# Kernel tuning notes

Hardware: AMD Instinct MI355X
Metric: run time of the kernel (lower is better)

Reference implementation:

```python
import jax, jax.numpy as jnp
import numpy as np

P = 100   # num_proxies
N = 1024  # num_samples
D = 512


def _edge_index():
    # complete bipartite proxy<->sample graph, both directions, plus self-loops
    # (PyG GATConv adds self-loops for all nodes by default)
    p = np.arange(P)
    s = np.arange(P, P + N)
    src_ps = np.repeat(p, N)   # proxy -> sample
    dst_ps = np.tile(s, P)
    loops = np.arange(P + N)
    src = np.concatenate([src_ps, dst_ps, loops]).astype(np.int32)
    dst = np.concatenate([dst_ps, src_ps, loops]).astype(np.int32)
    return jnp.asarray(src), jnp.asarray(dst)


def setup_inputs() -> dict:
    key = jax.random.key(0)
    ks = jax.random.split(key, 10)
    sc = 1.0 / np.sqrt(D)
    src, dst = _edge_index()
    return {
        "x": jax.random.normal(ks[0], (N, D), jnp.float32),
        "proxies": jax.random.normal(ks[1], (P, D), jnp.float32),
        "W1": jax.random.normal(ks[2], (D, D), jnp.float32) * sc,
        "a_src1": jax.random.normal(ks[3], (D,), jnp.float32) * sc,
        "a_dst1": jax.random.normal(ks[4], (D,), jnp.float32) * sc,
        "b1": jnp.zeros((D,), jnp.float32),
        "W2": jax.random.normal(ks[5], (D, D), jnp.float32) * sc,
        "a_src2": jax.random.normal(ks[6], (D,), jnp.float32) * sc,
        "a_dst2": jax.random.normal(ks[7], (D,), jnp.float32) * sc,
        "b2": jnp.zeros((D,), jnp.float32),
        "fc_w": jax.random.normal(ks[8], (D, 100), jnp.float32) * sc,
        "fc_b": jnp.zeros((100,), jnp.float32),
        "src": src,
        "dst": dst,
    }


def _gat_conv(x, src, dst, W, a_src, a_dst, b, n_nodes):
    # PyG GATConv, heads=1, concat=True, negative_slope=0.2
    h = x @ W                      # [n, D]
    l_src = h @ a_src              # [n]
    l_dst = h @ a_dst              # [n]
    e = jax.nn.leaky_relu(l_src[src] + l_dst[dst], 0.2)   # [E]
    # segment softmax over edges sharing the same destination
    e = e - jax.ops.segment_max(e, dst, num_segments=n_nodes)[dst]
    ex = jnp.exp(e)
    denom = jax.ops.segment_sum(ex, dst, num_segments=n_nodes)[dst]
    alpha = ex / denom             # [E]
    out = jax.ops.segment_sum(alpha[:, None] * h[src], dst, num_segments=n_nodes)
    return out + b


def reference(x, proxies, W1, a_src1, a_dst1, b1, W2, a_src2, a_dst2, b2, fc_w, fc_b, src, dst):
    n = P + N
    h = jnp.concatenate([proxies, x], axis=0)          # [P+N, D]
    h = jax.nn.relu(_gat_conv(h, src, dst, W1, a_src1, a_dst1, b1, n))
    # Dropout -> identity (eval)
    h = jax.nn.relu(_gat_conv(h, src, dst, W2, a_src2, a_dst2, b2, n))
    preds = h @ fc_w + fc_b                            # [P+N, 100]
    return preds[P:], h[P:]
```

## Files before the change

kernel.cpp:

```cpp
#include <hip/hip_runtime.h>

#define PP 100
#define NS 1024
#define NN 1124
#define DD 512
#define CC 100
#define NTHR 256

typedef _Float16 f16;
typedef _Float16 f16x8 __attribute__((ext_vector_type(8)));
typedef float    f32x4 __attribute__((ext_vector_type(4)));

__device__ __forceinline__ float lk(float v) { return v > 0.f ? v : 0.2f * v; }
__device__ __forceinline__ f16 hif(float v) { return (f16)v; }
__device__ __forceinline__ f16 lof(float v) { return (f16)(v - (float)((f16)v)); }

__device__ __forceinline__ void mgemm_core(
    const f16* __restrict__ Ah, const f16* __restrict__ Al,
    const f16* __restrict__ Bth, const f16* __restrict__ Btl,
    int K, int row0, int col0, f16* __restrict__ lds, f32x4 acc[2][2])
{
  const int t = threadIdx.x;
  const int lane = t & 63, w = t >> 6;
  const int wr = w >> 1, wc = w & 1;
  f16* Ash = lds;
  f16* Asl = lds + 2560;
  f16* Bsh = lds + 5120;
  f16* Bsl = lds + 7680;
  const int srow = t >> 2, su = t & 3;
  const size_t aoff = (size_t)(row0 + srow) * K + su * 8;
  const size_t boff = (size_t)(col0 + srow) * K + su * 8;
  const int lw = srow * 40 + su * 8;
  f32x4 pa0 = *(const f32x4*)(Ah + aoff);
  f32x4 pa1 = *(const f32x4*)(Al + aoff);
  f32x4 pb0 = *(const f32x4*)(Bth + boff);
  f32x4 pb1 = *(const f32x4*)(Btl + boff);
  const int fra = wr * 32 + (lane & 15);
  const int frb = wc * 32 + (lane & 15);
  const int fu  = (lane >> 4) * 8;
  for (int kt = 32; kt <= K; kt += 32) {
    *(f32x4*)(Ash + lw) = pa0;
    *(f32x4*)(Asl + lw) = pa1;
    *(f32x4*)(Bsh + lw) = pb0;
    *(f32x4*)(Bsl + lw) = pb1;
    __syncthreads();
    if (kt < K) {
      pa0 = *(const f32x4*)(Ah + aoff + kt);
      pa1 = *(const f32x4*)(Al + aoff + kt);
      pb0 = *(const f32x4*)(Bth + boff + kt);
      pb1 = *(const f32x4*)(Btl + boff + kt);
    }
    f16x8 ah[2], al[2], bh[2], bl[2];
#pragma unroll
    for (int m = 0; m < 2; ++m) {
      ah[m] = *(const f16x8*)(Ash + (fra + m * 16) * 40 + fu);
      al[m] = *(const f16x8*)(Asl + (fra + m * 16) * 40 + fu);
    }
#pragma unroll
    for (int n = 0; n < 2; ++n) {
      bh[n] = *(const f16x8*)(Bsh + (frb + n * 16) * 40 + fu);
      bl[n] = *(const f16x8*)(Bsl + (frb + n * 16) * 40 + fu);
    }
#pragma unroll
    for (int m = 0; m < 2; ++m)
#pragma unroll
      for (int n = 0; n < 2; ++n) {
        acc[m][n] = __builtin_amdgcn_mfma_f32_16x16x32_f16(ah[m], bh[n], acc[m][n], 0, 0, 0);
        acc[m][n] = __builtin_amdgcn_mfma_f32_16x16x32_f16(al[m], bh[n], acc[m][n], 0, 0, 0);
        acc[m][n] = __builtin_amdgcn_mfma_f32_16x16x32_f16(ah[m], bl[n], acc[m][n], 0, 0, 0);
      }
    __syncthreads();
  }
}


__device__ __forceinline__ void cvt_tile(
    const float* __restrict__ in, int R, int Cin,
    f16* __restrict__ oh, f16* __restrict__ ol, int ldo,
    int ti, int tj, f16 (*th)[72], f16 (*tl)[72])
{
  const int t = threadIdx.x;
#pragma unroll
  for (int p = 0; p < 4; ++p) {
    const int f = t + p * 256;
    const int i = f >> 4, j4 = (f & 15) * 4;
    const int gi = ti * 64 + i, gj = tj * 64 + j4;
    float4 v = make_float4(0.f, 0.f, 0.f, 0.f);
    if (gi < R && gj + 3 < Cin) v = *(const float4*)(in + (size_t)gi * Cin + gj);
    th[i][j4 + 0] = hif(v.x); tl[i][j4 + 0] = lof(v.x);
    th[i][j4 + 1] = hif(v.y); tl[i][j4 + 1] = lof(v.y);
    th[i][j4 + 2] = hif(v.z); tl[i][j4 + 2] = lof(v.z);
    th[i][j4 + 3] = hif(v.w); tl[i][j4 + 3] = lof(v.w);
  }
  __syncthreads();
#pragma unroll
  for (int p = 0; p < 2; ++p) {
    const int f = t + p * 256;
    const int j = f >> 3, i8 = (f & 7) * 8;
    f16x8 vh, vl;
#pragma unroll
    for (int e = 0; e < 8; ++e) { vh[e] = th[i8 + e][j]; vl[e] = tl[i8 + e][j]; }
    const size_t o = (size_t)(tj * 64 + j) * ldo + ti * 64 + i8;
    *(f16x8*)(oh + o) = vh;
    *(f16x8*)(ol + o) = vl;
  }
}

__global__ __launch_bounds__(NTHR) void prep_k(
    const float* __restrict__ x, const float* __restrict__ prox,
    const float* __restrict__ W1, const float* __restrict__ W2,
    const float* __restrict__ fcw,
    const float* __restrict__ as1, const float* __restrict__ ad1,
    const float* __restrict__ as2, const float* __restrict__ ad2,
    f16* xth, f16* xtl, f16* pth, f16* ptl,
    f16* W1th, f16* W1tl, f16* W2th, f16* W2tl, f16* fwth, f16* fwtl,
    float* v1s, float* v1d, float* v2s, float* v2d)
{
  __shared__ f16 th[64][72];
  __shared__ f16 tl[64][72];
  const int b = blockIdx.x;
  if (b < 64) {
    cvt_tile(W1, 512, 512, W1th, W1tl, 512, b >> 3, b & 7, th, tl);
  } else if (b < 128) {
    cvt_tile(W2, 512, 512, W2th, W2tl, 512, (b - 64) >> 3, (b - 64) & 7, th, tl);
  } else if (b < 256) {
    cvt_tile(x, NS, 512, xth, xtl, NS, (b - 128) >> 3, (b - 128) & 7, th, tl);
  } else if (b < 272) {
    cvt_tile(prox, PP, 512, pth, ptl, 128, (b - 256) >> 3, (b - 256) & 7, th, tl);
  } else if (b < 288) {
    cvt_tile(fcw, 512, CC, fwth, fwtl, 512, (b - 272) >> 1, (b - 272) & 1, th, tl);
  } else {
    const int wid  = (b - 288) * 4 + (threadIdx.x >> 6);
    const int lane = threadIdx.x & 63;
    const int r = wid & 511;
    const bool l1 = (wid < 512);
    const float* W = l1 ? W1 : W2;
    const float4* a4 = (const float4*)(l1 ? as1 : as2);
    const float4* b4 = (const float4*)(l1 ? ad1 : ad2);
    const float4* w4 = (const float4*)(W + (size_t)r * DD);
    float4 w0 = w4[lane], w1 = w4[lane + 64];
    float4 a0 = a4[lane], a1 = a4[lane + 64];
    float4 b0 = b4[lane], b1 = b4[lane + 64];
    float s1 = w0.x * a0.x + w0.y * a0.y + w0.z * a0.z + w0.w * a0.w
             + w1.x * a1.x + w1.y * a1.y + w1.z * a1.z + w1.w * a1.w;
    float s2 = w0.x * b0.x + w0.y * b0.y + w0.z * b0.z + w0.w * b0.w
             + w1.x * b1.x + w1.y * b1.y + w1.z * b1.z + w1.w * b1.w;
#pragma unroll
    for (int off = 32; off > 0; off >>= 1) {
      s1 += __shfl_down(s1, off);
      s2 += __shfl_down(s2, off);
    }
    if (lane == 0) {
      (l1 ? v1s : v2s)[r] = s1;
      (l1 ? v1d : v2d)[r] = s2;
    }
  }
}

__global__ __launch_bounds__(NTHR) void lvec_k(
    const float* __restrict__ A0, const float* __restrict__ A1, int split,
    const float* __restrict__ vs, const float* __restrict__ vd,
    float* __restrict__ ls, float* __restrict__ ld)
{
  const int r    = blockIdx.x * 4 + (threadIdx.x >> 6);
  const int lane = threadIdx.x & 63;
  if (r >= NN) return;
  const float* row = (r < split) ? A0 + (size_t)r * DD : A1 + (size_t)(r - split) * DD;
  const float4* r4 = (const float4*)row;
  const float4* s4 = (const float4*)vs;
  const float4* d4 = (const float4*)vd;
  float4 v0 = r4[lane], v1 = r4[lane + 64];
  float4 a0 = s4[lane], a1 = s4[lane + 64];
  float4 b0 = d4[lane], b1 = d4[lane + 64];
  float s1 = v0.x * a0.x + v0.y * a0.y + v0.z * a0.z + v0.w * a0.w
           + v1.x * a1.x + v1.y * a1.y + v1.z * a1.z + v1.w * a1.w;
  float s2 = v0.x * b0.x + v0.y * b0.y + v0.z * b0.z + v0.w * b0.w
           + v1.x * b1.x + v1.y * b1.y + v1.z * b1.z + v1.w * b1.w;
#pragma unroll
  for (int off = 32; off > 0; off >>= 1) {
    s1 += __shfl_down(s1, off);
    s2 += __shfl_down(s2, off);
  }
  if (lane == 0) { ls[r] = s1; ld[r] = s2; }
}

__global__ __launch_bounds__(NTHR) void alpha_k(
    const float* __restrict__ ls, const float* __restrict__ ld,
    f16* __restrict__ Esh, f16* __restrict__ Esl,
    float* __restrict__ esS, float* __restrict__ izS,
    f16* __restrict__ Eph, f16* __restrict__ Epl,
    float* __restrict__ esP, float* __restrict__ izP)
{
  const int t = threadIdx.x;
  if (blockIdx.x < 256) {
    const int lane = t & 63;
    const int i = blockIdx.x * 4 + (t >> 6);
    const float ldi = ld[PP + i];
    float e0 = lk(ls[lane] + ldi);
    float e1 = (lane < PP - 64) ? lk(ls[lane + 64] + ldi) : -1e30f;
    const float eself = lk(ls[PP + i] + ldi);
    float m = fmaxf(fmaxf(e0, e1), eself);
#pragma unroll
    for (int off = 1; off < 64; off <<= 1) m = fmaxf(m, __shfl_xor(m, off));
    float x0 = __expf(e0 - m);
    float x1 = (lane < PP - 64) ? __expf(e1 - m) : 0.f;
    float z = x0 + x1;
#pragma unroll
    for (int off = 1; off < 64; off <<= 1) z += __shfl_xor(z, off);
    Esh[(size_t)i * 128 + lane]      = hif(x0);
    Esl[(size_t)i * 128 + lane]      = lof(x0);
    Esh[(size_t)i * 128 + 64 + lane] = hif(x1);
    Esl[(size_t)i * 128 + 64 + lane] = lof(x1);
    if (lane == 0) {
      float xs = __expf(eself - m);
      esS[i] = xs;
      izS[i] = 1.f / (z + xs);
    }
  } else {
    const int i = blockIdx.x - 256;
    if (i >= PP) {
#pragma unroll
      for (int q = 0; q < 4; ++q) {
        Eph[(size_t)i * NS + t + q * 256] = (f16)0.f;
        Epl[(size_t)i * NS + t + q * 256] = (f16)0.f;
      }
      return;
    }
    __shared__ float red[4];
    const float ldi = ld[i];
    const float eself = lk(ls[i] + ldi);
    float e[4];
#pragma unroll
    for (int q = 0; q < 4; ++q) e[q] = lk(ls[PP + t + q * 256] + ldi);
    float m = fmaxf(fmaxf(fmaxf(e[0], e[1]), fmaxf(e[2], e[3])), eself);
#pragma unroll
    for (int off = 1; off < 64; off <<= 1) m = fmaxf(m, __shfl_xor(m, off));
    if ((t & 63) == 0) red[t >> 6] = m;
    __syncthreads();
    m = fmaxf(fmaxf(red[0], red[1]), fmaxf(red[2], red[3]));
    __syncthreads();
    float xq[4], z = 0.f;
#pragma unroll
    for (int q = 0; q < 4; ++q) { xq[q] = __expf(e[q] - m); z += xq[q]; }
#pragma unroll
    for (int off = 1; off < 64; off <<= 1) z += __shfl_xor(z, off);
    if ((t & 63) == 0) red[t >> 6] = z;
    __syncthreads();
#pragma unroll
    for (int q = 0; q < 4; ++q) {
      Eph[(size_t)i * NS + t + q * 256] = hif(xq[q]);
      Epl[(size_t)i * NS + t + q * 256] = lof(xq[q]);
    }
    if (t == 0) {
      float xs = __expf(eself - m);
      esP[i] = xs;
      izP[i] = 1.f / (red[0] + red[1] + red[2] + red[3] + xs);
    }
  }
}

__global__ __launch_bounds__(NTHR) void agg1_k(
    const f16* __restrict__ Es1h, const f16* __restrict__ Es1l,
    const f16* __restrict__ pth,  const f16* __restrict__ ptl,
    const f16* __restrict__ Eph,  const f16* __restrict__ Epl,
    const f16* __restrict__ xth,  const f16* __restrict__ xtl,
    const float* __restrict__ x, const float* __restrict__ prox,
    const float* __restrict__ esS, const float* __restrict__ izS,
    const float* __restrict__ esP, const float* __restrict__ izP,
    f16* __restrict__ M1h, f16* __restrict__ M1l)
{
  __shared__ __align__(16) f16 lds[10240];
  f32x4 acc[2][2] = {};
  const int t = threadIdx.x, lane = t & 63, w = t >> 6, wr = w >> 1, wc = w & 1;
  const int b = blockIdx.x;
  if (b < 128) {
    const int row0 = (b >> 3) * 64, col0 = (b & 7) * 64;
    mgemm_core(Es1h, Es1l, pth, ptl, 128, row0, col0, lds, acc);
#pragma unroll
    for (int m = 0; m < 2; ++m)
#pragma unroll
      for (int q = 0; q < 4; ++q) {
        const int r = row0 + wr * 32 + m * 16 + (lane >> 4) * 4 + q;
        const float e = esS[r], z = izS[r];
#pragma unroll
        for (int n = 0; n < 2; ++n) {
          const int c = col0 + wc * 32 + n * 16 + (lane & 15);
          const float v = (acc[m][n][q] + e * x[(size_t)r * DD + c]) * z;
          const size_t o = (size_t)(PP + r) * DD + c;
          M1h[o] = hif(v); M1l[o] = lof(v);
        }
      }
  } else {
    const int b2 = b - 128;
    const int row0 = (b2 >> 3) * 64, col0 = (b2 & 7) * 64;
    mgemm_core(Eph, Epl, xth, xtl, NS, row0, col0, lds, acc);
#pragma unroll
    for (int m = 0; m < 2; ++m)
#pragma unroll
      for (int q = 0; q < 4; ++q) {
        const int r = row0 + wr * 32 + m * 16 + (lane >> 4) * 4 + q;
        if (r < PP) {
          const float e = esP[r], z = izP[r];
#pragma unroll
          for (int n = 0; n < 2; ++n) {
            const int c = col0 + wc * 32 + n * 16 + (lane & 15);
            const float v = (acc[m][n][q] + e * prox[(size_t)r * DD + c]) * z;
            const size_t o = (size_t)r * DD + c;
            M1h[o] = hif(v); M1l[o] = lof(v);
          }
        }
      }
  }
}

__global__ __launch_bounds__(NTHR) void h1_k(
    const f16* __restrict__ M1h, const f16* __restrict__ M1l,
    const f16* __restrict__ W1th, const f16* __restrict__ W1tl,
    const float* __restrict__ b1, float* __restrict__ h1,
    f16* __restrict__ h1pth, f16* __restrict__ h1ptl)
{
  __shared__ __align__(16) f16 lds[10240];
  f32x4 acc[2][2] = {};
  const int t = threadIdx.x, lane = t & 63, w = t >> 6, wr = w >> 1, wc = w & 1;
  const int b = blockIdx.x;
  const int row0 = (b >> 3) * 64, col0 = (b & 7) * 64;
  mgemm_core(M1h, M1l, W1th, W1tl, DD, row0, col0, lds, acc);
#pragma unroll
  for (int m = 0; m < 2; ++m)
#pragma unroll
    for (int q = 0; q < 4; ++q) {
      const int r = row0 + wr * 32 + m * 16 + (lane >> 4) * 4 + q;
      if (r >= NN) continue;
#pragma unroll
      for (int n = 0; n < 2; ++n) {
        const int c = col0 + wc * 32 + n * 16 + (lane & 15);
        const float v = fmaxf(acc[m][n][q] + b1[c], 0.f);
        h1[(size_t)r * DD + c] = v;
        if (r < 128) {
          const size_t o = (size_t)c * 128 + r;
          f16 hh = (f16)0.f, ll = (f16)0.f;
          if (r < PP) { hh = hif(v); ll = lof(v); }
          h1pth[o] = hh; h1ptl[o] = ll;
        }
      }
    }
}

__global__ __launch_bounds__(NTHR) void agg2_k(
    const f16* __restrict__ Es2h, const f16* __restrict__ Es2l,
    const f16* __restrict__ h1pth, const f16* __restrict__ h1ptl,
    const float* __restrict__ h1,
    const float* __restrict__ esS, const float* __restrict__ izS,
    f16* __restrict__ M2h, f16* __restrict__ M2l)
{
  __shared__ __align__(16) f16 lds[10240];
  f32x4 acc[2][2] = {};
  const int t = threadIdx.x, lane = t & 63, w = t >> 6, wr = w >> 1, wc = w & 1;
  const int b = blockIdx.x;
  const int row0 = (b >> 3) * 64, col0 = (b & 7) * 64;
  mgemm_core(Es2h, Es2l, h1pth, h1ptl, 128, row0, col0, lds, acc);
#pragma unroll
  for (int m = 0; m < 2; ++m)
#pragma unroll
    for (int q = 0; q < 4; ++q) {
      const int r = row0 + wr * 32 + m * 16 + (lane >> 4) * 4 + q;
      const float e = esS[r], z = izS[r];
#pragma unroll
      for (int n = 0; n < 2; ++n) {
        const int c = col0 + wc * 32 + n * 16 + (lane & 15);
        const float v = (acc[m][n][q] + e * h1[(size_t)(PP + r) * DD + c]) * z;
        const size_t o = (size_t)r * DD + c;
        M2h[o] = hif(v); M2l[o] = lof(v);
      }
    }
}

__global__ __launch_bounds__(NTHR) void h2_k(
    const f16* __restrict__ M2h, const f16* __restrict__ M2l,
    const f16* __restrict__ W2th, const f16* __restrict__ W2tl,
    const float* __restrict__ b2, float* __restrict__ h2s,
    f16* __restrict__ h2h, f16* __restrict__ h2l)
{
  __shared__ __align__(16) f16 lds[10240];
  f32x4 acc[2][2] = {};
  const int t = threadIdx.x, lane = t & 63, w = t >> 6, wr = w >> 1, wc = w & 1;
  const int b = blockIdx.x;
  const int row0 = (b >> 3) * 64, col0 = (b & 7) * 64;
  mgemm_core(M2h, M2l, W2th, W2tl, DD, row0, col0, lds, acc);
#pragma unroll
  for (int m = 0; m < 2; ++m)
#pragma unroll
    for (int q = 0; q < 4; ++q) {
      const int r = row0 + wr * 32 + m * 16 + (lane >> 4) * 4 + q;
#pragma unroll
      for (int n = 0; n < 2; ++n) {
        const int c = col0 + wc * 32 + n * 16 + (lane & 15);
        const float v = fmaxf(acc[m][n][q] + b2[c], 0.f);
        const size_t o = (size_t)r * DD + c;
        h2s[o] = v;
        h2h[o] = hif(v); h2l[o] = lof(v);
      }
    }
}

__global__ __launch_bounds__(NTHR) void fc_k(
    const f16* __restrict__ h2h, const f16* __restrict__ h2l,
    const f16* __restrict__ fwth, const f16* __restrict__ fwtl,
    const float* __restrict__ fcb, float* __restrict__ out)
{
  __shared__ __align__(16) f16 lds[10240];
  f32x4 acc[2][2] = {};
  const int t = threadIdx.x, lane = t & 63, w = t >> 6, wr = w >> 1, wc = w & 1;
  const int b = blockIdx.x;
  const int row0 = (b >> 1) * 64, col0 = (b & 1) * 64;
  mgemm_core(h2h, h2l, fwth, fwtl, DD, row0, col0, lds, acc);
#pragma unroll
  for (int m = 0; m < 2; ++m)
#pragma unroll
    for (int q = 0; q < 4; ++q) {
      const int r = row0 + wr * 32 + m * 16 + (lane >> 4) * 4 + q;
#pragma unroll
      for (int n = 0; n < 2; ++n) {
        const int c = col0 + wc * 32 + n * 16 + (lane & 15);
        if (c < CC) out[(size_t)r * CC + c] = acc[m][n][q] + fcb[c];
      }
    }
}

extern "C" void kernel_launch(void* const* d_in, const int* in_sizes, int n_in,
                              void* d_out, int out_size, void* d_ws, size_t ws_size,
                              hipStream_t stream)
{
  const float* x    = (const float*)d_in[0];
  const float* prox = (const float*)d_in[1];
  const float* W1   = (const float*)d_in[2];
  const float* as1  = (const float*)d_in[3];
  const float* ad1  = (const float*)d_in[4];
  const float* b1   = (const float*)d_in[5];
  const float* W2   = (const float*)d_in[6];
  const float* as2  = (const float*)d_in[7];
  const float* ad2  = (const float*)d_in[8];
  const float* b2   = (const float*)d_in[9];
  const float* fcw  = (const float*)d_in[10];
  const float* fcb  = (const float*)d_in[11];
  float* out = (float*)d_out;

  float* F = (float*)d_ws;
  float* h1   = F; F += (size_t)NN * DD;
  float* ls1  = F; F += 1152;
  float* ld1  = F; F += 1152;
  float* ls2  = F; F += 1152;
  float* ld2  = F; F += 1152;
  float* v1s  = F; F += DD;
  float* v1d  = F; F += DD;
  float* v2s  = F; F += DD;
  float* v2d  = F; F += DD;
  float* esS1 = F; F += NS;
  float* izS1 = F; F += NS;
  float* esS2 = F; F += NS;
  float* izS2 = F; F += NS;
  float* esP  = F; F += 128;
  float* izP  = F; F += 128;
  f16* H = (f16*)F;
  f16* M1h  = H; H += (size_t)1152 * DD;
  f16* M1l  = H; H += (size_t)1152 * DD;
  f16* M2h  = H; H += (size_t)NS * DD;
  f16* M2l  = H; H += (size_t)NS * DD;
  f16* Es1h = H; H += (size_t)NS * 128;
  f16* Es1l = H; H += (size_t)NS * 128;
  f16* Es2h = H; H += (size_t)NS * 128;
  f16* Es2l = H; H += (size_t)NS * 128;
  f16* Eph  = H; H += (size_t)128 * NS;
  f16* Epl  = H; H += (size_t)128 * NS;
  f16* xth  = H; H += (size_t)DD * NS;
  f16* xtl  = H; H += (size_t)DD * NS;
  f16* pth  = H; H += (size_t)DD * 128;
  f16* ptl  = H; H += (size_t)DD * 128;
  f16* W1th = H; H += (size_t)DD * DD;
  f16* W1tl = H; H += (size_t)DD * DD;
  f16* W2th = H; H += (size_t)DD * DD;
  f16* W2tl = H; H += (size_t)DD * DD;
  f16* fwth = H; H += (size_t)128 * DD;
  f16* fwtl = H; H += (size_t)128 * DD;
  f16* h2h  = H; H += (size_t)NS * DD;
  f16* h2l  = H; H += (size_t)NS * DD;
  f16* h1pth = H; H += (size_t)DD * 128;
  f16* h1ptl = H; H += (size_t)DD * 128;
  float* h2s = out + (size_t)NS * CC;

  dim3 blk(NTHR);
  prep_k<<<dim3(544), blk, 0, stream>>>(x, prox, W1, W2, fcw, as1, ad1, as2, ad2,
      xth, xtl, pth, ptl, W1th, W1tl, W2th, W2tl, fwth, fwtl,
      v1s, v1d, v2s, v2d);
  lvec_k<<<dim3(281), blk, 0, stream>>>(prox, x, PP, v1s, v1d, ls1, ld1);
  alpha_k<<<dim3(256 + 128), blk, 0, stream>>>(ls1, ld1, Es1h, Es1l, esS1, izS1,
                                               Eph, Epl, esP, izP);
  agg1_k<<<dim3(144), blk, 0, stream>>>(Es1h, Es1l, pth, ptl, Eph, Epl, xth, xtl,
                                        x, prox, esS1, izS1, esP, izP, M1h, M1l);
  h1_k<<<dim3(144), blk, 0, stream>>>(M1h, M1l, W1th, W1tl, b1, h1, h1pth, h1ptl);
  lvec_k<<<dim3(281), blk, 0, stream>>>(h1, h1, NN, v2s, v2d, ls2, ld2);
  alpha_k<<<dim3(256), blk, 0, stream>>>(ls2, ld2, Es2h, Es2l, esS2, izS2,
                                         Eph, Epl, esP, izP);
  agg2_k<<<dim3(128), blk, 0, stream>>>(Es2h, Es2l, h1pth, h1ptl, h1,
                                        esS2, izS2, M2h, M2l);
  h2_k<<<dim3(128), blk, 0, stream>>>(M2h, M2l, W2th, W2tl, b2, h2s, h2h, h2l);
  fc_k<<<dim3(32), blk, 0, stream>>>(h2h, h2l, fwth, fwtl, fcb, out);
}
```

Baseline: 158.9 us.

## Fuse attention softmax into aggregation GEMMs and attention logits into GEMM epilogue

Removes the separate lvec and alpha kernels. Attention exponentials are now computed on the fly inside the aggregation GEMM's A-tile staging, using a global max bound instead of the exact per-row max. The layer-2 source and destination logits are accumulated in h1_k's epilogue via atomics, and the layer-1 logits are computed inside the prep kernel, which splits prep into two launches. This cuts launch count from 10 to 7 and drops the intermediate E matrices. In exchange it recomputes exp per block and adds atomic float adds, whose summation order is nondeterministic.

```diff
diff --git a/kernel.cpp b/kernel.cpp
--- a/kernel.cpp
+++ b/kernel.cpp
@@ -73,6 +73,121 @@
   }
 }
 
+__device__ __forceinline__ void agg_core(
+    const float* __restrict__ lsrc, int kvalid,
+    const float* __restrict__ ldb, const float* __restrict__ lsb,
+    const f16* __restrict__ Bth, const f16* __restrict__ Btl,
+    int K, int row0, int col0, int rvalid,
+    const float* __restrict__ selfv,
+    f16* __restrict__ outh, f16* __restrict__ outl,
+    f16* __restrict__ lds, float* __restrict__ fred)
+{
+  const int t = threadIdx.x, lane = t & 63, w = t >> 6;
+  const int wr = w >> 1, wc = w & 1;
+  f16* Ash = lds;
+  f16* Asl = lds + 2560;
+  f16* Bsh = lds + 5120;
+  f16* Bsl = lds + 7680;
+  float* zred = fred;
+  float* res  = fred + 256;
+  float* riz  = fred + 320;
+  const int srow = t >> 2, su = t & 3;
+  float sm = -1e30f;
+  for (int k = t; k < kvalid; k += NTHR) sm = fmaxf(sm, lsrc[k]);
+#pragma unroll
+  for (int off = 1; off < 64; off <<= 1) sm = fmaxf(sm, __shfl_xor(sm, off));
+  if (lane == 0) zred[w] = sm;
+  __syncthreads();
+  sm = fmaxf(fmaxf(zred[0], zred[1]), fmaxf(zred[2], zred[3]));
+  __syncthreads();
+  const bool rok = (row0 + srow) < rvalid;
+  float ldr = 0.f, mr = 0.f;
+  if (rok) {
+    ldr = ldb[row0 + srow];
+    mr  = lk(fmaxf(sm, lsb[row0 + srow]) + ldr);
+  }
+  const size_t boff = (size_t)(col0 + srow) * K + su * 8;
+  const int lw = srow * 40 + su * 8;
+  f32x4 pb0 = *(const f32x4*)(Bth + boff);
+  f32x4 pb1 = *(const f32x4*)(Btl + boff);
+  const int fra = wr * 32 + (lane & 15);
+  const int frb = wc * 32 + (lane & 15);
+  const int fu  = (lane >> 4) * 8;
+  f32x4 acc[2][2] = {};
+  float zacc = 0.f;
+  for (int kt = 32; kt <= K; kt += 32) {
+    f16x8 ae, al8;
+    const int k0 = kt - 32 + su * 8;
+#pragma unroll
+    for (int j = 0; j < 8; ++j) {
+      const int k = k0 + j;
+      float f = 0.f;
+      if (rok && k < kvalid) f = __expf(lk(lsrc[k] + ldr) - mr);
+      zacc += f;
+      ae[j]  = hif(f);
+      al8[j] = lof(f);
+    }
+    *(f16x8*)(Ash + lw) = ae;
+    *(f16x8*)(Asl + lw) = al8;
+    *(f32x4*)(Bsh + lw) = pb0;
+    *(f32x4*)(Bsl + lw) = pb1;
+    __syncthreads();
+    if (kt < K) {
+      pb0 = *(const f32x4*)(Bth + boff + kt);
+      pb1 = *(const f32x4*)(Btl + boff + kt);
+    }
+    f16x8 ah[2], alr[2], bh[2], bl[2];
+#pragma unroll
+    for (int m = 0; m < 2; ++m) {
+      ah[m]  = *(const f16x8*)(Ash + (fra + m * 16) * 40 + fu);
+      alr[m] = *(const f16x8*)(Asl + (fra + m * 16) * 40 + fu);
+    }
+#pragma unroll
+    for (int n = 0; n < 2; ++n) {
+      bh[n] = *(const f16x8*)(Bsh + (frb + n * 16) * 40 + fu);
+      bl[n] = *(const f16x8*)(Bsl + (frb + n * 16) * 40 + fu);
+    }
+#pragma unroll
+    for (int m = 0; m < 2; ++m)
+#pragma unroll
+      for (int n = 0; n < 2; ++n) {
+        acc[m][n] = __builtin_amdgcn_mfma_f32_16x16x32_f16(ah[m],  bh[n], acc[m][n], 0, 0, 0);
+        acc[m][n] = __builtin_amdgcn_mfma_f32_16x16x32_f16(alr[m], bh[n], acc[m][n], 0, 0, 0);
+        acc[m][n] = __builtin_amdgcn_mfma_f32_16x16x32_f16(ah[m],  bl[n], acc[m][n], 0, 0, 0);
+      }
+    __syncthreads();
+  }
+  zred[t] = zacc;
+  __syncthreads();
+  if (t < 64) {
+    float z = zred[t * 4] + zred[t * 4 + 1] + zred[t * 4 + 2] + zred[t * 4 + 3];
+    float es = 0.f, iz = 0.f;
+    if (row0 + t < rvalid) {
+      const float l2 = ldb[row0 + t], s2 = lsb[row0 + t];
+      const float m2 = lk(fmaxf(sm, s2) + l2);
+      es = __expf(lk(s2 + l2) - m2);
+      iz = 1.f / (z + es);
+    }
+    res[t] = es; riz[t] = iz;
+  }
+  __syncthreads();
+#pragma unroll
+  for (int m = 0; m < 2; ++m)
+#pragma unroll
+    for (int q = 0; q < 4; ++q) {
+      const int rl = wr * 32 + m * 16 + (lane >> 4) * 4 + q;
+      const int gr = row0 + rl;
+      if (gr >= rvalid) continue;
+      const float es = res[rl], iz = riz[rl];
+#pragma unroll
+      for (int n = 0; n < 2; ++n) {
+        const int c = col0 + wc * 32 + n * 16 + (lane & 15);
+        const float v = (acc[m][n][q] + es * selfv[(size_t)gr * DD + c]) * iz;
+        outh[(size_t)gr * DD + c] = hif(v);
+        outl[(size_t)gr * DD + c] = lof(v);
+      }
+    }
+}
 
 __device__ __forceinline__ void cvt_tile(
     const float* __restrict__ in, int R, int Cin,
@@ -106,15 +221,53 @@
   }
 }
 
-__global__ __launch_bounds__(NTHR) void prep_k(
+__global__ __launch_bounds__(NTHR) void prep1_k(
+    const float* __restrict__ W1, const float* __restrict__ W2,
+    const float* __restrict__ as1, const float* __restrict__ ad1,
+    const float* __restrict__ as2, const float* __restrict__ ad2,
+    float* __restrict__ v1s, float* __restrict__ v1d,
+    float* __restrict__ v2s, float* __restrict__ v2d,
+    float* __restrict__ ls2, float* __restrict__ ld2)
+{
+  const int u = blockIdx.x;
+  if (u < 256) {
+    const int wid  = u * 4 + (threadIdx.x >> 6);
+    const int lane = threadIdx.x & 63;
+    const int r = wid & 511;
+    const bool l1 = (wid < 512);
+    const float* W = l1 ? W1 : W2;
+    const float4* a4 = (const float4*)(l1 ? as1 : as2);
+    const float4* b4 = (const float4*)(l1 ? ad1 : ad2);
+    const float4* w4 = (const float4*)(W + (size_t)r * DD);
+    float4 w0 = w4[lane], w1 = w4[lane + 64];
+    float4 a0 = a4[lane], a1 = a4[lane + 64];
+    float4 b0 = b4[lane], b1 = b4[lane + 64];
+    float s1 = w0.x * a0.x + w0.y * a0.y + w0.z * a0.z + w0.w * a0.w
+             + w1.x * a1.x + w1.y * a1.y + w1.z * a1.z + w1.w * a1.w;
+    float s2 = w0.x * b0.x + w0.y * b0.y + w0.z * b0.z + w0.w * b0.w
+             + w1.x * b1.x + w1.y * b1.y + w1.z * b1.z + w1.w * b1.w;
+#pragma unroll
+    for (int off = 32; off > 0; off >>= 1) {
+      s1 += __shfl_down(s1, off);
+      s2 += __shfl_down(s2, off);
+    }
+    if (lane == 0) {
+      (l1 ? v1s : v2s)[r] = s1;
+      (l1 ? v1d : v2d)[r] = s2;
+    }
+  } else {
+    for (int i = threadIdx.x; i < 1152; i += NTHR) { ls2[i] = 0.f; ld2[i] = 0.f; }
+  }
+}
+
+__global__ __launch_bounds__(NTHR) void prep2_k(
     const float* __restrict__ x, const float* __restrict__ prox,
     const float* __restrict__ W1, const float* __restrict__ W2,
     const float* __restrict__ fcw,
-    const float* __restrict__ as1, const float* __restrict__ ad1,
-    const float* __restrict__ as2, const float* __restrict__ ad2,
+    const float* __restrict__ v1s, const float* __restrict__ v1d,
     f16* xth, f16* xtl, f16* pth, f16* ptl,
     f16* W1th, f16* W1tl, f16* W2th, f16* W2tl, f16* fwth, f16* fwtl,
-    float* v1s, float* v1d, float* v2s, float* v2d)
+    float* __restrict__ ls1, float* __restrict__ ld1)
 {
   __shared__ f16 th[64][72];
   __shared__ f16 tl[64][72];
@@ -130,194 +283,59 @@
   } else if (b < 288) {
     cvt_tile(fcw, 512, CC, fwth, fwtl, 512, (b - 272) >> 1, (b - 272) & 1, th, tl);
   } else {
-    const int wid  = (b - 288) * 4 + (threadIdx.x >> 6);
+    const int r    = (b - 288) * 4 + (threadIdx.x >> 6);
     const int lane = threadIdx.x & 63;
-    const int r = wid & 511;
-    const bool l1 = (wid < 512);
-    const float* W = l1 ? W1 : W2;
-    const float4* a4 = (const float4*)(l1 ? as1 : as2);
-    const float4* b4 = (const float4*)(l1 ? ad1 : ad2);
-    const float4* w4 = (const float4*)(W + (size_t)r * DD);
-    float4 w0 = w4[lane], w1 = w4[lane + 64];
-    float4 a0 = a4[lane], a1 = a4[lane + 64];
-    float4 b0 = b4[lane], b1 = b4[lane + 64];
-    float s1 = w0.x * a0.x + w0.y * a0.y + w0.z * a0.z + w0.w * a0.w
-             + w1.x * a1.x + w1.y * a1.y + w1.z * a1.z + w1.w * a1.w;
-    float s2 = w0.x * b0.x + w0.y * b0.y + w0.z * b0.z + w0.w * b0.w
-             + w1.x * b1.x + w1.y * b1.y + w1.z * b1.z + w1.w * b1.w;
+    if (r >= NN) return;
+    const float* row = (r < PP) ? prox + (size_t)r * DD
+                                : x + (size_t)(r - PP) * DD;
+    const float4* r4 = (const float4*)row;
+    const float4* s4 = (const float4*)v1s;
+    const float4* d4 = (const float4*)v1d;
+    float4 v0 = r4[lane], v1 = r4[lane + 64];
+    float4 a0 = s4[lane], a1 = s4[lane + 64];
+    float4 b0 = d4[lane], b1 = d4[lane + 64];
+    float s1 = v0.x * a0.x + v0.y * a0.y + v0.z * a0.z + v0.w * a0.w
+             + v1.x * a1.x + v1.y * a1.y + v1.z * a1.z + v1.w * a1.w;
+    float s2 = v0.x * b0.x + v0.y * b0.y + v0.z * b0.z + v0.w * b0.w
+             + v1.x * b1.x + v1.y * b1.y + v1.z * b1.z + v1.w * b1.w;
 #pragma unroll
     for (int off = 32; off > 0; off >>= 1) {
       s1 += __shfl_down(s1, off);
       s2 += __shfl_down(s2, off);
     }
-    if (lane == 0) {
-      (l1 ? v1s : v2s)[r] = s1;
-      (l1 ? v1d : v2d)[r] = s2;
-    }
-  }
-}
-
-__global__ __launch_bounds__(NTHR) void lvec_k(
-    const float* __restrict__ A0, const float* __restrict__ A1, int split,
-    const float* __restrict__ vs, const float* __restrict__ vd,
-    float* __restrict__ ls, float* __restrict__ ld)
-{
-  const int r    = blockIdx.x * 4 + (threadIdx.x >> 6);
-  const int lane = threadIdx.x & 63;
-  if (r >= NN) return;
-  const float* row = (r < split) ? A0 + (size_t)r * DD : A1 + (size_t)(r - split) * DD;
-  const float4* r4 = (const float4*)row;
-  const float4* s4 = (const float4*)vs;
-  const float4* d4 = (const float4*)vd;
-  float4 v0 = r4[lane], v1 = r4[lane + 64];
-  float4 a0 = s4[lane], a1 = s4[lane + 64];
-  float4 b0 = d4[lane], b1 = d4[lane + 64];
-  float s1 = v0.x * a0.x + v0.y * a0.y + v0.z * a0.z + v0.w * a0.w
-           + v1.x * a1.x + v1.y * a1.y + v1.z * a1.z + v1.w * a1.w;
-  float s2 = v0.x * b0.x + v0.y * b0.y + v0.z * b0.z + v0.w * b0.w
-           + v1.x * b1.x + v1.y * b1.y + v1.z * b1.z + v1.w * b1.w;
-#pragma unroll
-  for (int off = 32; off > 0; off >>= 1) {
-    s1 += __shfl_down(s1, off);
-    s2 += __shfl_down(s2, off);
-  }
-  if (lane == 0) { ls[r] = s1; ld[r] = s2; }
-}
-
-__global__ __launch_bounds__(NTHR) void alpha_k(
-    const float* __restrict__ ls, const float* __restrict__ ld,
-    f16* __restrict__ Esh, f16* __restrict__ Esl,
-    float* __restrict__ esS, float* __restrict__ izS,
-    f16* __restrict__ Eph, f16* __restrict__ Epl,
-    float* __restrict__ esP, float* __restrict__ izP)
-{
-  const int t = threadIdx.x;
-  if (blockIdx.x < 256) {
-    const int lane = t & 63;
-    const int i = blockIdx.x * 4 + (t >> 6);
-    const float ldi = ld[PP + i];
-    float e0 = lk(ls[lane] + ldi);
-    float e1 = (lane < PP - 64) ? lk(ls[lane + 64] + ldi) : -1e30f;
-    const float eself = lk(ls[PP + i] + ldi);
-    float m = fmaxf(fmaxf(e0, e1), eself);
-#pragma unroll
-    for (int off = 1; off < 64; off <<= 1) m = fmaxf(m, __shfl_xor(m, off));
-    float x0 = __expf(e0 - m);
-    float x1 = (lane < PP - 64) ? __expf(e1 - m) : 0.f;
-    float z = x0 + x1;
-#pragma unroll
-    for (int off = 1; off < 64; off <<= 1) z += __shfl_xor(z, off);
-    Esh[(size_t)i * 128 + lane]      = hif(x0);
-    Esl[(size_t)i * 128 + lane]      = lof(x0);
-    Esh[(size_t)i * 128 + 64 + lane] = hif(x1);
-    Esl[(size_t)i * 128 + 64 + lane] = lof(x1);
-    if (lane == 0) {
-      float xs = __expf(eself - m);
-      esS[i] = xs;
-      izS[i] = 1.f / (z + xs);
-    }
-  } else {
-    const int i = blockIdx.x - 256;
-    if (i >= PP) {
-#pragma unroll
-      for (int q = 0; q < 4; ++q) {
-        Eph[(size_t)i * NS + t + q * 256] = (f16)0.f;
-        Epl[(size_t)i * NS + t + q * 256] = (f16)0.f;
-      }
-      return;
-    }
-    __shared__ float red[4];
-    const float ldi = ld[i];
-    const float eself = lk(ls[i] + ldi);
-    float e[4];
-#pragma unroll
-    for (int q = 0; q < 4; ++q) e[q] = lk(ls[PP + t + q * 256] + ldi);
-    float m = fmaxf(fmaxf(fmaxf(e[0], e[1]), fmaxf(e[2], e[3])), eself);
-#pragma unroll
-    for (int off = 1; off < 64; off <<= 1) m = fmaxf(m, __shfl_xor(m, off));
-    if ((t & 63) == 0) red[t >> 6] = m;
-    __syncthreads();
-    m = fmaxf(fmaxf(red[0], red[1]), fmaxf(red[2], red[3]));
-    __syncthreads();
-    float xq[4], z = 0.f;
-#pragma unroll
-    for (int q = 0; q < 4; ++q) { xq[q] = __expf(e[q] - m); z += xq[q]; }
-#pragma unroll
-    for (int off = 1; off < 64; off <<= 1) z += __shfl_xor(z, off);
-    if ((t & 63) == 0) red[t >> 6] = z;
-    __syncthreads();
-#pragma unroll
-    for (int q = 0; q < 4; ++q) {
-      Eph[(size_t)i * NS + t + q * 256] = hif(xq[q]);
-      Epl[(size_t)i * NS + t + q * 256] = lof(xq[q]);
-    }
-    if (t == 0) {
-      float xs = __expf(eself - m);
-      esP[i] = xs;
-      izP[i] = 1.f / (red[0] + red[1] + red[2] + red[3] + xs);
-    }
-  }
-}
-
-__global__ __launch_bounds__(NTHR) void agg1_k(
-    const f16* __restrict__ Es1h, const f16* __restrict__ Es1l,
-    const f16* __restrict__ pth,  const f16* __restrict__ ptl,
-    const f16* __restrict__ Eph,  const f16* __restrict__ Epl,
-    const f16* __restrict__ xth,  const f16* __restrict__ xtl,
+    if (lane == 0) { ls1[r] = s1; ld1[r] = s2; }
+  }
+}
+
+__global__ __launch_bounds__(NTHR) void agg1x_k(
+    const float* __restrict__ ls1, const float* __restrict__ ld1,
+    const f16* __restrict__ pth, const f16* __restrict__ ptl,
+    const f16* __restrict__ xth, const f16* __restrict__ xtl,
     const float* __restrict__ x, const float* __restrict__ prox,
-    const float* __restrict__ esS, const float* __restrict__ izS,
-    const float* __restrict__ esP, const float* __restrict__ izP,
     f16* __restrict__ M1h, f16* __restrict__ M1l)
 {
   __shared__ __align__(16) f16 lds[10240];
-  f32x4 acc[2][2] = {};
-  const int t = threadIdx.x, lane = t & 63, w = t >> 6, wr = w >> 1, wc = w & 1;
+  __shared__ float fred[384];
   const int b = blockIdx.x;
   if (b < 128) {
     const int row0 = (b >> 3) * 64, col0 = (b & 7) * 64;
-    mgemm_core(Es1h, Es1l, pth, ptl, 128, row0, col0, lds, acc);
-#pragma unroll
-    for (int m = 0; m < 2; ++m)
-#pragma unroll
-      for (int q = 0; q < 4; ++q) {
-        const int r = row0 + wr * 32 + m * 16 + (lane >> 4) * 4 + q;
-        const float e = esS[r], z = izS[r];
-#pragma unroll
-        for (int n = 0; n < 2; ++n) {
-          const int c = col0 + wc * 32 + n * 16 + (lane & 15);
-          const float v = (acc[m][n][q] + e * x[(size_t)r * DD + c]) * z;
-          const size_t o = (size_t)(PP + r) * DD + c;
-          M1h[o] = hif(v); M1l[o] = lof(v);
-        }
-      }
+    agg_core(ls1, PP, ld1 + PP, ls1 + PP, pth, ptl, 128, row0, col0, NS,
+             x, M1h + (size_t)PP * DD, M1l + (size_t)PP * DD, lds, fred);
   } else {
     const int b2 = b - 128;
     const int row0 = (b2 >> 3) * 64, col0 = (b2 & 7) * 64;
-    mgemm_core(Eph, Epl, xth, xtl, NS, row0, col0, lds, acc);
-#pragma unroll
-    for (int m = 0; m < 2; ++m)
-#pragma unroll
-      for (int q = 0; q < 4; ++q) {
-        const int r = row0 + wr * 32 + m * 16 + (lane >> 4) * 4 + q;
-        if (r < PP) {
-          const float e = esP[r], z = izP[r];
-#pragma unroll
-          for (int n = 0; n < 2; ++n) {
-            const int c = col0 + wc * 32 + n * 16 + (lane & 15);
-            const float v = (acc[m][n][q] + e * prox[(size_t)r * DD + c]) * z;
-            const size_t o = (size_t)r * DD + c;
-            M1h[o] = hif(v); M1l[o] = lof(v);
-          }
-        }
-      }
+    agg_core(ls1 + PP, NS, ld1, ls1, xth, xtl, NS, row0, col0, PP,
+             prox, M1h, M1l, lds, fred);
   }
 }
 
 __global__ __launch_bounds__(NTHR) void h1_k(
     const f16* __restrict__ M1h, const f16* __restrict__ M1l,
     const f16* __restrict__ W1th, const f16* __restrict__ W1tl,
-    const float* __restrict__ b1, float* __restrict__ h1,
-    f16* __restrict__ h1pth, f16* __restrict__ h1ptl)
+    const float* __restrict__ b1,
+    const float* __restrict__ v2s, const float* __restrict__ v2d,
+    float* __restrict__ h1, f16* __restrict__ h1pth, f16* __restrict__ h1ptl,
+    float* __restrict__ ls2, float* __restrict__ ld2)
 {
   __shared__ __align__(16) f16 lds[10240];
   f32x4 acc[2][2] = {};
@@ -325,17 +343,25 @@
   const int b = blockIdx.x;
   const int row0 = (b >> 3) * 64, col0 = (b & 7) * 64;
   mgemm_core(M1h, M1l, W1th, W1tl, DD, row0, col0, lds, acc);
+  const int c0 = col0 + wc * 32 + (lane & 15);
+  const int c1 = c0 + 16;
+  const float vs0 = v2s[c0], vs1 = v2s[c1];
+  const float vd0 = v2d[c0], vd1 = v2d[c1];
+  const float bb0 = b1[c0],  bb1 = b1[c1];
 #pragma unroll
   for (int m = 0; m < 2; ++m)
 #pragma unroll
     for (int q = 0; q < 4; ++q) {
       const int r = row0 + wr * 32 + m * 16 + (lane >> 4) * 4 + q;
       if (r >= NN) continue;
+      float ps = 0.f, pd = 0.f;
 #pragma unroll
       for (int n = 0; n < 2; ++n) {
-        const int c = col0 + wc * 32 + n * 16 + (lane & 15);
-        const float v = fmaxf(acc[m][n][q] + b1[c], 0.f);
+        const int c = (n == 0) ? c0 : c1;
+        const float v = fmaxf(acc[m][n][q] + (n == 0 ? bb0 : bb1), 0.f);
         h1[(size_t)r * DD + c] = v;
+        ps += v * (n == 0 ? vs0 : vs1);
+        pd += v * (n == 0 ? vd0 : vd1);
         if (r < 128) {
           const size_t o = (size_t)c * 128 + r;
           f16 hh = (f16)0.f, ll = (f16)0.f;
@@ -343,36 +369,30 @@
           h1pth[o] = hh; h1ptl[o] = ll;
         }
       }
-    }
-}
-
-__global__ __launch_bounds__(NTHR) void agg2_k(
-    const f16* __restrict__ Es2h, const f16* __restrict__ Es2l,
+#pragma unroll
+      for (int off = 1; off < 16; off <<= 1) {
+        ps += __shfl_xor(ps, off);
+        pd += __shfl_xor(pd, off);
+      }
+      if ((lane & 15) == 0) {
+        atomicAdd(&ls2[r], ps);
+        atomicAdd(&ld2[r], pd);
+      }
+    }
+}
+
+__global__ __launch_bounds__(NTHR) void agg2x_k(
+    const float* __restrict__ ls2, const float* __restrict__ ld2,
     const f16* __restrict__ h1pth, const f16* __restrict__ h1ptl,
     const float* __restrict__ h1,
-    const float* __restrict__ esS, const float* __restrict__ izS,
     f16* __restrict__ M2h, f16* __restrict__ M2l)
 {
   __shared__ __align__(16) f16 lds[10240];
-  f32x4 acc[2][2] = {};
-  const int t = threadIdx.x, lane = t & 63, w = t >> 6, wr = w >> 1, wc = w & 1;
+  __shared__ float fred[384];
   const int b = blockIdx.x;
   const int row0 = (b >> 3) * 64, col0 = (b & 7) * 64;
-  mgemm_core(Es2h, Es2l, h1pth, h1ptl, 128, row0, col0, lds, acc);
-#pragma unroll
-  for (int m = 0; m < 2; ++m)
-#pragma unroll
-    for (int q = 0; q < 4; ++q) {
-      const int r = row0 + wr * 32 + m * 16 + (lane >> 4) * 4 + q;
-      const float e = esS[r], z = izS[r];
-#pragma unroll
-      for (int n = 0; n < 2; ++n) {
-        const int c = col0 + wc * 32 + n * 16 + (lane & 15);
-        const float v = (acc[m][n][q] + e * h1[(size_t)(PP + r) * DD + c]) * z;
-        const size_t o = (size_t)r * DD + c;
-        M2h[o] = hif(v); M2l[o] = lof(v);
-      }
-    }
+  agg_core(ls2, PP, ld2 + PP, ls2 + PP, h1pth, h1ptl, 128, row0, col0, NS,
+           h1 + (size_t)PP * DD, M2h, M2l, lds, fred);
 }
 
 __global__ __launch_bounds__(NTHR) void h2_k(
@@ -455,23 +475,11 @@
   float* v1d  = F; F += DD;
   float* v2s  = F; F += DD;
   float* v2d  = F; F += DD;
-  float* esS1 = F; F += NS;
-  float* izS1 = F; F += NS;
-  float* esS2 = F; F += NS;
-  float* izS2 = F; F += NS;
-  float* esP  = F; F += 128;
-  float* izP  = F; F += 128;
   f16* H = (f16*)F;
   f16* M1h  = H; H += (size_t)1152 * DD;
   f16* M1l  = H; H += (size_t)1152 * DD;
   f16* M2h  = H; H += (size_t)NS * DD;
   f16* M2l  = H; H += (size_t)NS * DD;
-  f16* Es1h = H; H += (size_t)NS * 128;
-  f16* Es1l = H; H += (size_t)NS * 128;
-  f16* Es2h = H; H += (size_t)NS * 128;
-  f16* Es2l = H; H += (size_t)NS * 128;
-  f16* Eph  = H; H += (size_t)128 * NS;
-  f16* Epl  = H; H += (size_t)128 * NS;
   f16* xth  = H; H += (size_t)DD * NS;
   f16* xtl  = H; H += (size_t)DD * NS;
   f16* pth  = H; H += (size_t)DD * 128;
@@ -489,20 +497,15 @@
   float* h2s = out + (size_t)NS * CC;
 
   dim3 blk(NTHR);
-  prep_k<<<dim3(544), blk, 0, stream>>>(x, prox, W1, W2, fcw, as1, ad1, as2, ad2,
-      xth, xtl, pth, ptl, W1th, W1tl, W2th, W2tl, fwth, fwtl,
-      v1s, v1d, v2s, v2d);
-  lvec_k<<<dim3(281), blk, 0, stream>>>(prox, x, PP, v1s, v1d, ls1, ld1);
-  alpha_k<<<dim3(256 + 128), blk, 0, stream>>>(ls1, ld1, Es1h, Es1l, esS1, izS1,
-                                               Eph, Epl, esP, izP);
-  agg1_k<<<dim3(144), blk, 0, stream>>>(Es1h, Es1l, pth, ptl, Eph, Epl, xth, xtl,
-                                        x, prox, esS1, izS1, esP, izP, M1h, M1l);
-  h1_k<<<dim3(144), blk, 0, stream>>>(M1h, M1l, W1th, W1tl, b1, h1, h1pth, h1ptl);
-  lvec_k<<<dim3(281), blk, 0, stream>>>(h1, h1, NN, v2s, v2d, ls2, ld2);
-  alpha_k<<<dim3(256), blk, 0, stream>>>(ls2, ld2, Es2h, Es2l, esS2, izS2,
-                                         Eph, Epl, esP, izP);
-  agg2_k<<<dim3(128), blk, 0, stream>>>(Es2h, Es2l, h1pth, h1ptl, h1,
-                                        esS2, izS2, M2h, M2l);
+  prep1_k<<<dim3(257), blk, 0, stream>>>(W1, W2, as1, ad1, as2, ad2,
+                                         v1s, v1d, v2s, v2d, ls2, ld2);
+  prep2_k<<<dim3(569), blk, 0, stream>>>(x, prox, W1, W2, fcw, v1s, v1d,
+      xth, xtl, pth, ptl, W1th, W1tl, W2th, W2tl, fwth, fwtl, ls1, ld1);
+  agg1x_k<<<dim3(144), blk, 0, stream>>>(ls1, ld1, pth, ptl, xth, xtl,
+                                         x, prox, M1h, M1l);
+  h1_k<<<dim3(144), blk, 0, stream>>>(M1h, M1l, W1th, W1tl, b1, v2s, v2d,
+                                      h1, h1pth, h1ptl, ls2, ld2);
+  agg2x_k<<<dim3(128), blk, 0, stream>>>(ls2, ld2, h1pth, h1ptl, h1, M2h, M2l);
   h2_k<<<dim3(128), blk, 0, stream>>>(M2h, M2l, W2th, W2tl, b2, h2s, h2h, h2l);
   fc_k<<<dim3(32), blk, 0, stream>>>(h2h, h2l, fwth, fwtl, fcb, out);
 }
```

Measured after the change: 178.1 us. 1.12x slower.
